# Kernel tuning notes

Hardware: AMD Instinct MI355X
Metric: run time of the kernel (lower is better)

## Reference

```python
import jax, jax.numpy as jnp
import numpy as np

NUM_HEADS = 8  # matches init_kwargs


def setup_inputs() -> dict:
    key = jax.random.key(0)
    ks = jax.random.split(key, 8)
    B, S, E = 2, 512, 256
    inp = {
        "query": jax.random.normal(ks[0], (B, S, E), dtype=jnp.float32),
        "key": jax.random.normal(ks[1], (B, S, E), dtype=jnp.float32),
        "value": jax.random.normal(ks[2], (B, S, E), dtype=jnp.float32),
        "relations": jax.random.randint(ks[3], (B, S, S), 0, 33, dtype=jnp.int64),
        "W_Q": jax.random.normal(ks[4], (E, E), dtype=jnp.float32) * (E ** -0.5),
        "W_K": jax.random.normal(ks[5], (E, E), dtype=jnp.float32) * (E ** -0.5),
        "W_V": jax.random.normal(ks[6], (E, E), dtype=jnp.float32) * (E ** -0.5),
        "rel_emb": jax.random.normal(ks[7], (33, E), dtype=jnp.float32),
    }
    return inp


def reference(query, key, value, relations, W_Q, W_K, W_V, rel_emb):
    B, S, E = query.shape
    H = NUM_HEADS
    D = E // H
    scale = 1.0 / np.sqrt(D).astype(np.float32)

    # Projections (torch Linear: x @ W.T), split heads -> [B,S,H,D]
    q = (query @ W_Q.T).reshape(B, S, H, D)
    k = (key @ W_K.T).reshape(B, S, H, D)
    v = (value @ W_V.T).reshape(B, S, H, D)

    # Per-pair relation bias r[b,i,j] -> [B,S,S,H,D]
    rh = rel_emb[relations].reshape(B, S, S, H, D)

    # Faithful to original indexing: scores[b,h,i,j] = q_i . (K_i + r_{ij}) / sqrt(D)
    # Split into the (j-independent) q.K_i diagonal term plus the relation term,
    # avoiding materializing the [B,S,S,H,D] K+r tensor.
    qk_diag = jnp.einsum("bihd,bihd->bhi", q, k)  # [B,H,S]
    scores = (qk_diag[..., None] + jnp.einsum("bihd,bijhd->bhij", q, rh)) * scale
    alpha = jax.nn.softmax(scores, axis=-1)  # [B,H,S,S]

    # z[b,i,h] = sum_j alpha[b,h,i,j] * (V_i + r_{ij})
    alpha_sum = jnp.einsum("bhij->bih", alpha)  # == 1, kept for faithfulness
    z = v * alpha_sum[..., None] + jnp.einsum("bhij,bijhd->bihd", alpha, rh)
    return z.reshape(B, S, E)
```

## Files before the change

kernel.cpp:

```cpp
#include <hip/hip_runtime.h>
#include <math.h>

namespace {
constexpr int E_  = 256;
constexpr int H_  = 8;
constexpr int D_  = 32;
constexpr int S_  = 512;
constexpr int NR_ = 33;
constexpr int RC_ = 32;
constexpr int ROWS_ = 1024;
}

using f32x4 = __attribute__((ext_vector_type(4))) float;
using s16x8 = __attribute__((ext_vector_type(8))) short;

__device__ inline unsigned pk_bf16(float a, float b) {
    unsigned ua = __float_as_uint(a); ua += 0x7FFFu + ((ua >> 16) & 1u);
    unsigned ub = __float_as_uint(b); ub += 0x7FFFu + ((ub >> 16) & 1u);
    return (ua >> 16) | (ub & 0xFFFF0000u);
}
__device__ inline unsigned short bf16_1(float a) {
    unsigned ua = __float_as_uint(a); ua += 0x7FFFu + ((ua >> 16) & 1u);
    return (unsigned short)(ua >> 16);
}

__device__ inline int swz(int row, int kbyte) {
    return row * 128 + (kbyte ^ ((row & 7) << 4));
}

__device__ inline void bar_lgkm() {
    asm volatile("s_waitcnt lgkmcnt(0)" ::: "memory");
    __builtin_amdgcn_s_barrier();
    __builtin_amdgcn_sched_barrier(0);
}

__global__ __launch_bounds__(256) void fused_kernel(
    const float* __restrict__ q_in, const float* __restrict__ v_in,
    const float* __restrict__ WQ,  const float* __restrict__ WV,
    const int*   __restrict__ relations,
    const float* __restrict__ rel_emb,
    float* __restrict__ out)
{
    __shared__ __align__(16) char  tiles[4][RC_ * 128];
    __shared__ __align__(16) float v_s[RC_][36];
    __shared__ __align__(16) unsigned short qbf_s[RC_ * 32];
    __shared__ __align__(16) float emb_s[NR_ * D_];
    __shared__ __align__(16) unsigned short ebf_s[48 * 32];
    __shared__ float qr_s[RC_][52];
    __shared__ int   cnt_s[RC_ * NR_];

    const int t  = threadIdx.x;
    const int r0 = blockIdx.x * RC_;
    const int h  = blockIdx.y;
    const int c0 = h * D_;

    float4 pre[16];
    auto issue = [&](int kt, int buf) {
        #pragma unroll
        for (int j = 0; j < 8; ++j) {
            const int tau = j >> 1;
            const int idx = t + 256 * (j & 1);
            const int row = idx >> 4;
            const int cf  = (idx & 15) * 4;
            const float* src = (tau == 0) ? q_in : (tau == 1) ? v_in
                             : (tau == 2) ? WQ   : WV;
            const int rb = (tau < 2) ? r0 : c0;
            pre[buf * 8 + j] = *reinterpret_cast<const float4*>(
                &src[(size_t)(rb + row) * E_ + kt * 64 + cf]);
        }
    };
    auto wtiles = [&](int buf) {
        #pragma unroll
        for (int j = 0; j < 8; ++j) {
            const int tau = j >> 1;
            const int idx = t + 256 * (j & 1);
            const int row = idx >> 4;
            const int cb  = (idx & 15) * 8;
            const float4 p = pre[buf * 8 + j];
            *reinterpret_cast<uint2*>(tiles[tau] + swz(row, cb)) =
                make_uint2(pk_bf16(p.x, p.y), pk_bf16(p.z, p.w));
        }
    };

    issue(0, 0);
    issue(1, 1);
    const int hrow = t >> 3, hl = t & 7;
    int4 rel[16];
    {
        const int* relrow = relations + (size_t)(r0 + hrow) * S_;
        #pragma unroll
        for (int i = 0; i < 16; ++i)
            rel[i] = *reinterpret_cast<const int4*>(&relrow[hl * 4 + i * 32]);
    }
    for (int i = t; i < RC_ * NR_; i += 256) cnt_s[i] = 0;
    for (int g = t; g < NR_ * D_ / 4; g += 256) {
        const int r = g >> 3, d4 = (g & 7) * 4;
        const float4 ev = *reinterpret_cast<const float4*>(
            &rel_emb[(size_t)r * E_ + c0 + d4]);
        *reinterpret_cast<float4*>(&emb_s[r * D_ + d4]) = ev;
        *reinterpret_cast<uint2*>(&ebf_s[r * 32 + d4]) =
            make_uint2(pk_bf16(ev.x, ev.y), pk_bf16(ev.z, ev.w));
    }
    for (int i = t; i < (48 - NR_) * 32 / 2; i += 256)
        reinterpret_cast<unsigned*>(ebf_s + NR_ * 32)[i] = 0;
    bar_lgkm();

    const int l  = t & 63;
    const int w  = t >> 6;
    const int mi = (w >> 1) * 16;
    const int ni = (w & 1) * 16;
    const int lr = l & 15;
    const int lk = (l >> 4) * 16;

    f32x4 accq = {}, accv = {};

    #pragma unroll
    for (int kt = 0; kt < 4; ++kt) {
        wtiles(kt & 1);
        if (kt < 2) issue(kt + 2, kt & 1);
        bar_lgkm();
        #pragma unroll
        for (int s = 0; s < 2; ++s) {
            const int kb = s * 64 + lk;
            const s16x8 aq = *reinterpret_cast<const s16x8*>(tiles[0] + swz(mi + lr, kb));
            const s16x8 av = *reinterpret_cast<const s16x8*>(tiles[1] + swz(mi + lr, kb));
            const s16x8 bq = *reinterpret_cast<const s16x8*>(tiles[2] + swz(ni + lr, kb));
            const s16x8 bv = *reinterpret_cast<const s16x8*>(tiles[3] + swz(ni + lr, kb));
            accq = __builtin_amdgcn_mfma_f32_16x16x32_bf16(aq, bq, accq, 0, 0, 0);
            accv = __builtin_amdgcn_mfma_f32_16x16x32_bf16(av, bv, accv, 0, 0, 0);
        }
        #pragma unroll
        for (int i = 0; i < 4; ++i) {
            const int4 rv = rel[kt * 4 + i];
            atomicAdd(&cnt_s[hrow * NR_ + rv.x], 1);
            atomicAdd(&cnt_s[hrow * NR_ + rv.y], 1);
            atomicAdd(&cnt_s[hrow * NR_ + rv.z], 1);
            atomicAdd(&cnt_s[hrow * NR_ + rv.w], 1);
        }
        bar_lgkm();
    }

    #pragma unroll
    for (int j = 0; j < 4; ++j) {
        const int row = mi + (l >> 4) * 4 + j;
        const int col = ni + lr;
        v_s[row][col] = accv[j];
        qbf_s[row * 32 + col] = bf16_1(accq[j]);
    }
    bar_lgkm();

    {
        const int kq = (l >> 4) * 8;
        const int Hh = w >> 1;
        const int G  = w & 1;
        const s16x8 afr = *reinterpret_cast<const s16x8*>(&qbf_s[(Hh * 16 + lr) * 32 + kq]);
        const s16x8 bfr = *reinterpret_cast<const s16x8*>(&ebf_s[(G  * 16 + lr) * 32 + kq]);
        f32x4 r1 = {};
        r1 = __builtin_amdgcn_mfma_f32_16x16x32_bf16(afr, bfr, r1, 0, 0, 0);
        #pragma unroll
        for (int j = 0; j < 4; ++j)
            qr_s[Hh * 16 + (l >> 4) * 4 + j][G * 16 + lr] = r1[j];
        if ((w & 1) == 0) {
            const s16x8 bf2 = *reinterpret_cast<const s16x8*>(&ebf_s[(32 + lr) * 32 + kq]);
            f32x4 r2 = {};
            r2 = __builtin_amdgcn_mfma_f32_16x16x32_bf16(afr, bf2, r2, 0, 0, 0);
            #pragma unroll
            for (int j = 0; j < 4; ++j)
                qr_s[Hh * 16 + (l >> 4) * 4 + j][32 + lr] = r2[j];
        }
    }
    bar_lgkm();

    const int erow = t >> 3, el = t & 7;
    {
        constexpr float scale = 0.17677669529663687f;
        float z[5], m = -1e30f;
        #pragma unroll
        for (int u = 0; u < 5; ++u) {
            const int r = el + 8 * u;
            z[u] = (r < NR_) ? qr_s[erow][r] * scale : -1e30f;
            m = fmaxf(m, z[u]);
        }
        m = fmaxf(m, __shfl_xor(m, 1));
        m = fmaxf(m, __shfl_xor(m, 2));
        m = fmaxf(m, __shfl_xor(m, 4));
        float e[5], sum = 0.f;
        #pragma unroll
        for (int u = 0; u < 5; ++u) {
            const int r = el + 8 * u;
            e[u] = (r < NR_) ? (float)cnt_s[erow * NR_ + r] * __expf(z[u] - m) : 0.f;
            sum += e[u];
        }
        sum += __shfl_xor(sum, 1);
        sum += __shfl_xor(sum, 2);
        sum += __shfl_xor(sum, 4);
        const float inv = 1.0f / sum;
        #pragma unroll
        for (int u = 0; u < 5; ++u) {
            const int r = el + 8 * u;
            if (r < NR_) qr_s[erow][r] = e[u] * inv;
        }
    }
    bar_lgkm();

    {
        const int d0 = el * 4;
        f32x4 acc = *reinterpret_cast<const f32x4*>(&v_s[erow][d0]);
        #pragma unroll
        for (int r = 0; r < NR_; ++r) {
            const float wv = qr_s[erow][r];
            const f32x4 ev = *reinterpret_cast<const f32x4*>(&emb_s[r * D_ + d0]);
            acc[0] += wv * ev[0]; acc[1] += wv * ev[1];
            acc[2] += wv * ev[2]; acc[3] += wv * ev[3];
        }
        *reinterpret_cast<f32x4*>(&out[(size_t)(r0 + erow) * E_ + c0 + d0]) = acc;
    }
}

extern "C" void kernel_launch(void* const* d_in, const int* in_sizes, int n_in,
                              void* d_out, int out_size, void* d_ws, size_t ws_size,
                              hipStream_t stream) {
    const float* query     = (const float*)d_in[0];
    const float* value     = (const float*)d_in[2];
    const int*   relations = (const int*)  d_in[3];
    const float* W_Q       = (const float*)d_in[4];
    const float* W_V       = (const float*)d_in[6];
    const float* rel_emb   = (const float*)d_in[7];
    float* out = (float*)d_out;

    dim3 grid(ROWS_ / RC_, H_);
    fused_kernel<<<grid, 256, 0, stream>>>(query, value, W_Q, W_V,
                                           relations, rel_emb, out);
}
```

Before: 12.49 us.

## Load projection MFMA fragments directly from global and broadcast softmax weights via shuffles

```diff
diff --git a/kernel.cpp b/kernel.cpp
--- a/kernel.cpp
+++ b/kernel.cpp
@@ -3,12 +3,12 @@
 
 namespace {
 constexpr int E_  = 256;
-constexpr int H_  = 8;
 constexpr int D_  = 32;
 constexpr int S_  = 512;
 constexpr int NR_ = 33;
 constexpr int RC_ = 32;
 constexpr int ROWS_ = 1024;
+constexpr int H_  = 8;
 }
 
 using f32x4 = __attribute__((ext_vector_type(4))) float;
@@ -23,9 +23,11 @@
     unsigned ua = __float_as_uint(a); ua += 0x7FFFu + ((ua >> 16) & 1u);
     return (unsigned short)(ua >> 16);
 }
-
-__device__ inline int swz(int row, int kbyte) {
-    return row * 128 + (kbyte ^ ((row & 7) << 4));
+__device__ inline s16x8 cvt8(const float4 a, const float4 b) {
+    union { unsigned u[4]; s16x8 v; } r;
+    r.u[0] = pk_bf16(a.x, a.y); r.u[1] = pk_bf16(a.z, a.w);
+    r.u[2] = pk_bf16(b.x, b.y); r.u[3] = pk_bf16(b.z, b.w);
+    return r.v;
 }
 
 __device__ inline void bar_lgkm() {
@@ -41,12 +43,11 @@
     const float* __restrict__ rel_emb,
     float* __restrict__ out)
 {
-    __shared__ __align__(16) char  tiles[4][RC_ * 128];
     __shared__ __align__(16) float v_s[RC_][36];
     __shared__ __align__(16) unsigned short qbf_s[RC_ * 32];
     __shared__ __align__(16) float emb_s[NR_ * D_];
     __shared__ __align__(16) unsigned short ebf_s[48 * 32];
-    __shared__ float qr_s[RC_][52];
+    __shared__ float qr_s[RC_][48];
     __shared__ int   cnt_s[RC_ * NR_];
 
     const int t  = threadIdx.x;
@@ -54,36 +55,13 @@
     const int h  = blockIdx.y;
     const int c0 = h * D_;
 
-    float4 pre[16];
-    auto issue = [&](int kt, int buf) {
-        #pragma unroll
-        for (int j = 0; j < 8; ++j) {
-            const int tau = j >> 1;
-            const int idx = t + 256 * (j & 1);
-            const int row = idx >> 4;
-            const int cf  = (idx & 15) * 4;
-            const float* src = (tau == 0) ? q_in : (tau == 1) ? v_in
-                             : (tau == 2) ? WQ   : WV;
-            const int rb = (tau < 2) ? r0 : c0;
-            pre[buf * 8 + j] = *reinterpret_cast<const float4*>(
-                &src[(size_t)(rb + row) * E_ + kt * 64 + cf]);
-        }
-    };
-    auto wtiles = [&](int buf) {
-        #pragma unroll
-        for (int j = 0; j < 8; ++j) {
-            const int tau = j >> 1;
-            const int idx = t + 256 * (j & 1);
-            const int row = idx >> 4;
-            const int cb  = (idx & 15) * 8;
-            const float4 p = pre[buf * 8 + j];
-            *reinterpret_cast<uint2*>(tiles[tau] + swz(row, cb)) =
-                make_uint2(pk_bf16(p.x, p.y), pk_bf16(p.z, p.w));
-        }
-    };
-
-    issue(0, 0);
-    issue(1, 1);
+    const int l  = t & 63;
+    const int w  = t >> 6;
+    const int mi = (w >> 1) * 16;
+    const int ni = (w & 1) * 16;
+    const int lr = l & 15;
+    const int lg = l >> 4;
+
     const int hrow = t >> 3, hl = t & 7;
     int4 rel[16];
     {
@@ -92,7 +70,7 @@
         for (int i = 0; i < 16; ++i)
             rel[i] = *reinterpret_cast<const int4*>(&relrow[hl * 4 + i * 32]);
     }
-    for (int i = t; i < RC_ * NR_; i += 256) cnt_s[i] = 0;
+
     for (int g = t; g < NR_ * D_ / 4; g += 256) {
         const int r = g >> 3, d4 = (g & 7) * 4;
         const float4 ev = *reinterpret_cast<const float4*>(
@@ -101,48 +79,41 @@
         *reinterpret_cast<uint2*>(&ebf_s[r * 32 + d4]) =
             make_uint2(pk_bf16(ev.x, ev.y), pk_bf16(ev.z, ev.w));
     }
-    for (int i = t; i < (48 - NR_) * 32 / 2; i += 256)
-        reinterpret_cast<unsigned*>(ebf_s + NR_ * 32)[i] = 0;
+    for (int i = t; i < RC_ * NR_; i += 256) cnt_s[i] = 0;
     bar_lgkm();
 
-    const int l  = t & 63;
-    const int w  = t >> 6;
-    const int mi = (w >> 1) * 16;
-    const int ni = (w & 1) * 16;
-    const int lr = l & 15;
-    const int lk = (l >> 4) * 16;
+    const float* qrow = q_in + (size_t)(r0 + mi + lr) * E_ + lg * 8;
+    const float* vrow = v_in + (size_t)(r0 + mi + lr) * E_ + lg * 8;
+    const float* wqr  = WQ   + (size_t)(c0 + ni + lr) * E_ + lg * 8;
+    const float* wvr  = WV   + (size_t)(c0 + ni + lr) * E_ + lg * 8;
 
     f32x4 accq = {}, accv = {};
-
     #pragma unroll
-    for (int kt = 0; kt < 4; ++kt) {
-        wtiles(kt & 1);
-        if (kt < 2) issue(kt + 2, kt & 1);
-        bar_lgkm();
-        #pragma unroll
-        for (int s = 0; s < 2; ++s) {
-            const int kb = s * 64 + lk;
-            const s16x8 aq = *reinterpret_cast<const s16x8*>(tiles[0] + swz(mi + lr, kb));
-            const s16x8 av = *reinterpret_cast<const s16x8*>(tiles[1] + swz(mi + lr, kb));
-            const s16x8 bq = *reinterpret_cast<const s16x8*>(tiles[2] + swz(ni + lr, kb));
-            const s16x8 bv = *reinterpret_cast<const s16x8*>(tiles[3] + swz(ni + lr, kb));
-            accq = __builtin_amdgcn_mfma_f32_16x16x32_bf16(aq, bq, accq, 0, 0, 0);
-            accv = __builtin_amdgcn_mfma_f32_16x16x32_bf16(av, bv, accv, 0, 0, 0);
-        }
-        #pragma unroll
-        for (int i = 0; i < 4; ++i) {
-            const int4 rv = rel[kt * 4 + i];
-            atomicAdd(&cnt_s[hrow * NR_ + rv.x], 1);
-            atomicAdd(&cnt_s[hrow * NR_ + rv.y], 1);
-            atomicAdd(&cnt_s[hrow * NR_ + rv.z], 1);
-            atomicAdd(&cnt_s[hrow * NR_ + rv.w], 1);
-        }
-        bar_lgkm();
+    for (int ks = 0; ks < 8; ++ks) {
+        const float4* q4 = reinterpret_cast<const float4*>(qrow + ks * 32);
+        const float4* v4 = reinterpret_cast<const float4*>(vrow + ks * 32);
+        const float4* a4 = reinterpret_cast<const float4*>(wqr  + ks * 32);
+        const float4* b4 = reinterpret_cast<const float4*>(wvr  + ks * 32);
+        const s16x8 aq = cvt8(q4[0], q4[1]);
+        const s16x8 av = cvt8(v4[0], v4[1]);
+        const s16x8 bq = cvt8(a4[0], a4[1]);
+        const s16x8 bv = cvt8(b4[0], b4[1]);
+        accq = __builtin_amdgcn_mfma_f32_16x16x32_bf16(aq, bq, accq, 0, 0, 0);
+        accv = __builtin_amdgcn_mfma_f32_16x16x32_bf16(av, bv, accv, 0, 0, 0);
+    }
+
+    #pragma unroll
+    for (int i = 0; i < 16; ++i) {
+        const int4 rv = rel[i];
+        atomicAdd(&cnt_s[hrow * NR_ + rv.x], 1);
+        atomicAdd(&cnt_s[hrow * NR_ + rv.y], 1);
+        atomicAdd(&cnt_s[hrow * NR_ + rv.z], 1);
+        atomicAdd(&cnt_s[hrow * NR_ + rv.w], 1);
     }
 
     #pragma unroll
     for (int j = 0; j < 4; ++j) {
-        const int row = mi + (l >> 4) * 4 + j;
+        const int row = mi + lg * 4 + j;
         const int col = ni + lr;
         v_s[row][col] = accv[j];
         qbf_s[row * 32 + col] = bf16_1(accq[j]);
@@ -150,7 +121,7 @@
     bar_lgkm();
 
     {
-        const int kq = (l >> 4) * 8;
+        const int kq = lg * 8;
         const int Hh = w >> 1;
         const int G  = w & 1;
         const s16x8 afr = *reinterpret_cast<const s16x8*>(&qbf_s[(Hh * 16 + lr) * 32 + kq]);
@@ -159,19 +130,21 @@
         r1 = __builtin_amdgcn_mfma_f32_16x16x32_bf16(afr, bfr, r1, 0, 0, 0);
         #pragma unroll
         for (int j = 0; j < 4; ++j)
-            qr_s[Hh * 16 + (l >> 4) * 4 + j][G * 16 + lr] = r1[j];
+            qr_s[Hh * 16 + lg * 4 + j][G * 16 + lr] = r1[j];
         if ((w & 1) == 0) {
             const s16x8 bf2 = *reinterpret_cast<const s16x8*>(&ebf_s[(32 + lr) * 32 + kq]);
             f32x4 r2 = {};
             r2 = __builtin_amdgcn_mfma_f32_16x16x32_bf16(afr, bf2, r2, 0, 0, 0);
             #pragma unroll
             for (int j = 0; j < 4; ++j)
-                qr_s[Hh * 16 + (l >> 4) * 4 + j][32 + lr] = r2[j];
+                qr_s[Hh * 16 + lg * 4 + j][32 + lr] = r2[j];
         }
     }
     bar_lgkm();
 
     const int erow = t >> 3, el = t & 7;
+    float e[5];
+    float inv;
     {
         constexpr float scale = 0.17677669529663687f;
         float z[5], m = -1e30f;
@@ -184,7 +157,7 @@
         m = fmaxf(m, __shfl_xor(m, 1));
         m = fmaxf(m, __shfl_xor(m, 2));
         m = fmaxf(m, __shfl_xor(m, 4));
-        float e[5], sum = 0.f;
+        float sum = 0.f;
         #pragma unroll
         for (int u = 0; u < 5; ++u) {
             const int r = el + 8 * u;
@@ -194,21 +167,15 @@
         sum += __shfl_xor(sum, 1);
         sum += __shfl_xor(sum, 2);
         sum += __shfl_xor(sum, 4);
-        const float inv = 1.0f / sum;
-        #pragma unroll
-        for (int u = 0; u < 5; ++u) {
-            const int r = el + 8 * u;
-            if (r < NR_) qr_s[erow][r] = e[u] * inv;
-        }
-    }
-    bar_lgkm();
-
+        inv = 1.0f / sum;
+    }
     {
         const int d0 = el * 4;
         f32x4 acc = *reinterpret_cast<const f32x4*>(&v_s[erow][d0]);
+        const int base = l & 56;
         #pragma unroll
         for (int r = 0; r < NR_; ++r) {
-            const float wv = qr_s[erow][r];
+            const float wv = __shfl(e[r >> 3], base | (r & 7)) * inv;
             const f32x4 ev = *reinterpret_cast<const f32x4*>(&emb_s[r * D_ + d0]);
             acc[0] += wv * ev[0]; acc[1] += wv * ev[1];
             acc[2] += wv * ev[2]; acc[3] += wv * ev[3];
```

Result: slower. 17.15 us (+37.3%).

## Double-buffer LDS tiles, drop a barrier, broadcast softmax weights via shuffles

Applied to the files above, without the earlier changes.

```diff
diff --git a/kernel.cpp b/kernel.cpp
--- a/kernel.cpp
+++ b/kernel.cpp
@@ -3,12 +3,12 @@
 
 namespace {
 constexpr int E_  = 256;
-constexpr int H_  = 8;
 constexpr int D_  = 32;
 constexpr int S_  = 512;
 constexpr int NR_ = 33;
 constexpr int RC_ = 32;
 constexpr int ROWS_ = 1024;
+constexpr int H_  = 8;
 }
 
 using f32x4 = __attribute__((ext_vector_type(4))) float;
@@ -41,7 +41,7 @@
     const float* __restrict__ rel_emb,
     float* __restrict__ out)
 {
-    __shared__ __align__(16) char  tiles[4][RC_ * 128];
+    __shared__ __align__(16) char  tiles[2][4][RC_ * 128];
     __shared__ __align__(16) float v_s[RC_][36];
     __shared__ __align__(16) unsigned short qbf_s[RC_ * 32];
     __shared__ __align__(16) float emb_s[NR_ * D_];
@@ -54,8 +54,15 @@
     const int h  = blockIdx.y;
     const int c0 = h * D_;
 
-    float4 pre[16];
-    auto issue = [&](int kt, int buf) {
+    const int l  = t & 63;
+    const int w  = t >> 6;
+    const int mi = (w >> 1) * 16;
+    const int ni = (w & 1) * 16;
+    const int lr = l & 15;
+    const int lk = (l >> 4) * 16;
+
+    float4 pre[2][8];
+    auto issue = [&](int kt, int slot) {
         #pragma unroll
         for (int j = 0; j < 8; ++j) {
             const int tau = j >> 1;
@@ -65,20 +72,34 @@
             const float* src = (tau == 0) ? q_in : (tau == 1) ? v_in
                              : (tau == 2) ? WQ   : WV;
             const int rb = (tau < 2) ? r0 : c0;
-            pre[buf * 8 + j] = *reinterpret_cast<const float4*>(
+            pre[slot][j] = *reinterpret_cast<const float4*>(
                 &src[(size_t)(rb + row) * E_ + kt * 64 + cf]);
         }
     };
-    auto wtiles = [&](int buf) {
+    auto wtiles = [&](int slot, int buf) {
         #pragma unroll
         for (int j = 0; j < 8; ++j) {
             const int tau = j >> 1;
             const int idx = t + 256 * (j & 1);
             const int row = idx >> 4;
             const int cb  = (idx & 15) * 8;
-            const float4 p = pre[buf * 8 + j];
-            *reinterpret_cast<uint2*>(tiles[tau] + swz(row, cb)) =
+            const float4 p = pre[slot][j];
+            *reinterpret_cast<uint2*>(tiles[buf][tau] + swz(row, cb)) =
                 make_uint2(pk_bf16(p.x, p.y), pk_bf16(p.z, p.w));
+        }
+    };
+
+    f32x4 accq = {}, accv = {};
+    auto mfma_tile = [&](int buf) {
+        #pragma unroll
+        for (int s = 0; s < 2; ++s) {
+            const int kb = s * 64 + lk;
+            const s16x8 aq = *reinterpret_cast<const s16x8*>(tiles[buf][0] + swz(mi + lr, kb));
+            const s16x8 av = *reinterpret_cast<const s16x8*>(tiles[buf][1] + swz(mi + lr, kb));
+            const s16x8 bq = *reinterpret_cast<const s16x8*>(tiles[buf][2] + swz(ni + lr, kb));
+            const s16x8 bv = *reinterpret_cast<const s16x8*>(tiles[buf][3] + swz(ni + lr, kb));
+            accq = __builtin_amdgcn_mfma_f32_16x16x32_bf16(aq, bq, accq, 0, 0, 0);
+            accv = __builtin_amdgcn_mfma_f32_16x16x32_bf16(av, bv, accv, 0, 0, 0);
         }
     };
 
@@ -92,7 +113,16 @@
         for (int i = 0; i < 16; ++i)
             rel[i] = *reinterpret_cast<const int4*>(&relrow[hl * 4 + i * 32]);
     }
-    for (int i = t; i < RC_ * NR_; i += 256) cnt_s[i] = 0;
+    auto hist = [&](int c) {
+        #pragma unroll
+        for (int i = 0; i < 4; ++i) {
+            const int4 rv = rel[c * 4 + i];
+            atomicAdd(&cnt_s[hrow * NR_ + rv.x], 1);
+            atomicAdd(&cnt_s[hrow * NR_ + rv.y], 1);
+            atomicAdd(&cnt_s[hrow * NR_ + rv.z], 1);
+            atomicAdd(&cnt_s[hrow * NR_ + rv.w], 1);
+        }
+    };
     for (int g = t; g < NR_ * D_ / 4; g += 256) {
         const int r = g >> 3, d4 = (g & 7) * 4;
         const float4 ev = *reinterpret_cast<const float4*>(
@@ -101,44 +131,26 @@
         *reinterpret_cast<uint2*>(&ebf_s[r * 32 + d4]) =
             make_uint2(pk_bf16(ev.x, ev.y), pk_bf16(ev.z, ev.w));
     }
-    for (int i = t; i < (48 - NR_) * 32 / 2; i += 256)
-        reinterpret_cast<unsigned*>(ebf_s + NR_ * 32)[i] = 0;
-    bar_lgkm();
-
-    const int l  = t & 63;
-    const int w  = t >> 6;
-    const int mi = (w >> 1) * 16;
-    const int ni = (w & 1) * 16;
-    const int lr = l & 15;
-    const int lk = (l >> 4) * 16;
-
-    f32x4 accq = {}, accv = {};
-
-    #pragma unroll
-    for (int kt = 0; kt < 4; ++kt) {
-        wtiles(kt & 1);
-        if (kt < 2) issue(kt + 2, kt & 1);
-        bar_lgkm();
-        #pragma unroll
-        for (int s = 0; s < 2; ++s) {
-            const int kb = s * 64 + lk;
-            const s16x8 aq = *reinterpret_cast<const s16x8*>(tiles[0] + swz(mi + lr, kb));
-            const s16x8 av = *reinterpret_cast<const s16x8*>(tiles[1] + swz(mi + lr, kb));
-            const s16x8 bq = *reinterpret_cast<const s16x8*>(tiles[2] + swz(ni + lr, kb));
-            const s16x8 bv = *reinterpret_cast<const s16x8*>(tiles[3] + swz(ni + lr, kb));
-            accq = __builtin_amdgcn_mfma_f32_16x16x32_bf16(aq, bq, accq, 0, 0, 0);
-            accv = __builtin_amdgcn_mfma_f32_16x16x32_bf16(av, bv, accv, 0, 0, 0);
-        }
-        #pragma unroll
-        for (int i = 0; i < 4; ++i) {
-            const int4 rv = rel[kt * 4 + i];
-            atomicAdd(&cnt_s[hrow * NR_ + rv.x], 1);
-            atomicAdd(&cnt_s[hrow * NR_ + rv.y], 1);
-            atomicAdd(&cnt_s[hrow * NR_ + rv.z], 1);
-            atomicAdd(&cnt_s[hrow * NR_ + rv.w], 1);
-        }
-        bar_lgkm();
-    }
+    if (t < 240) reinterpret_cast<unsigned*>(ebf_s + 33 * 32)[t] = 0;
+    for (int i = t; i < RC_ * NR_; i += 256) cnt_s[i] = 0;
+
+    wtiles(0, 0);
+    issue(2, 0);
+    bar_lgkm();
+
+    wtiles(1, 1);  issue(3, 1);
+    mfma_tile(0);  hist(0);
+    bar_lgkm();
+
+    wtiles(0, 0);
+    mfma_tile(1);  hist(1);
+    bar_lgkm();
+
+    wtiles(1, 1);
+    mfma_tile(0);  hist(2);
+    bar_lgkm();
+
+    mfma_tile(1);  hist(3);
 
     #pragma unroll
     for (int j = 0; j < 4; ++j) {
@@ -171,7 +183,9 @@
     }
     bar_lgkm();
 
-    const int erow = t >> 3, el = t & 7;
+    const int erow = hrow, el = hl;
+    float e[5];
+    float inv;
     {
         constexpr float scale = 0.17677669529663687f;
         float z[5], m = -1e30f;
@@ -184,7 +198,7 @@
         m = fmaxf(m, __shfl_xor(m, 1));
         m = fmaxf(m, __shfl_xor(m, 2));
         m = fmaxf(m, __shfl_xor(m, 4));
-        float e[5], sum = 0.f;
+        float sum = 0.f;
         #pragma unroll
         for (int u = 0; u < 5; ++u) {
             const int r = el + 8 * u;
@@ -194,21 +208,15 @@
         sum += __shfl_xor(sum, 1);
         sum += __shfl_xor(sum, 2);
         sum += __shfl_xor(sum, 4);
-        const float inv = 1.0f / sum;
-        #pragma unroll
-        for (int u = 0; u < 5; ++u) {
-            const int r = el + 8 * u;
-            if (r < NR_) qr_s[erow][r] = e[u] * inv;
-        }
-    }
-    bar_lgkm();
-
+        inv = 1.0f / sum;
+    }
     {
         const int d0 = el * 4;
         f32x4 acc = *reinterpret_cast<const f32x4*>(&v_s[erow][d0]);
+        const int base = l & 56;
         #pragma unroll
         for (int r = 0; r < NR_; ++r) {
-            const float wv = qr_s[erow][r];
+            const float wv = __shfl(e[r >> 3], base | (r & 7)) * inv;
             const f32x4 ev = *reinterpret_cast<const f32x4*>(&emb_s[r * D_ + d0]);
             acc[0] += wv * ev[0]; acc[1] += wv * ev[1];
             acc[2] += wv * ev[2]; acc[3] += wv * ev[3];
```

After: 12.46 us. About the same (-0.3%).
